# Performance work log

Hardware: AMD Instinct MI355X
Metric: run time of the kernel (lower is better)

Reference implementation:

```python
import jax, jax.numpy as jnp
import numpy as np

WINDOW_SIZE = 11
SIGMA = 1.5
C1 = 0.01 ** 2
C2 = 0.03 ** 2


def _gaussian_window(channels):
    coords = jnp.arange(WINDOW_SIZE, dtype=jnp.float32) - WINDOW_SIZE // 2
    g = jnp.exp(-coords ** 2 / (2.0 * SIGMA ** 2))
    g = g / g.sum()
    w2d = g[:, None] * g[None, :]                      # [K, K]
    # depthwise kernel: [out_ch=C, in_ch/groups=1, K, K]
    return jnp.broadcast_to(w2d[None, None], (channels, 1, WINDOW_SIZE, WINDOW_SIZE))


def _depthwise_conv(x, window):
    # x: [B, C, H, W]; grouped conv with feature_group_count = C, SAME padding
    C = x.shape[1]
    pad = WINDOW_SIZE // 2
    return jax.lax.conv_general_dilated(
        x, window,
        window_strides=(1, 1),
        padding=((pad, pad), (pad, pad)),
        dimension_numbers=("NCHW", "OIHW", "NCHW"),
        feature_group_count=C,
    )


def setup_inputs() -> dict:
    key = jax.random.key(0)
    k1, k2 = jax.random.split(key)
    shape = (16, 3, 512, 512)
    pred = jax.random.uniform(k1, shape, dtype=jnp.float32)
    target = jax.random.uniform(k2, shape, dtype=jnp.float32)
    return {"pred": pred, "target": target}


def reference(pred, target):
    C = pred.shape[1]
    window = _gaussian_window(C)
    mu_p = _depthwise_conv(pred, window)
    mu_t = _depthwise_conv(target, window)
    mu_p_sq = mu_p ** 2
    mu_t_sq = mu_t ** 2
    mu_cross = mu_p * mu_t
    sigma_p_sq = _depthwise_conv(pred ** 2, window) - mu_p_sq
    sigma_t_sq = _depthwise_conv(target ** 2, window) - mu_t_sq
    sigma_cross = _depthwise_conv(pred * target, window) - mu_cross
    ssim_map = ((2.0 * mu_cross + C1) * (2.0 * sigma_cross + C2)) / (
        (mu_p_sq + mu_t_sq + C1) * (sigma_p_sq + sigma_t_sq + C2)
    )
    return 1.0 - ssim_map.mean()
```

## Files before the change

kernel.cpp:

```cpp
#include <hip/hip_runtime.h>

#define HH 512
#define WW 512
#define NPLANE 48
#define BY 128
#define CHK 16
#define NCH (BY / CHK)
#define SLOTS 40
#define KS 11

typedef __attribute__((ext_vector_type(8))) short short8;
typedef __attribute__((ext_vector_type(4))) float floatx4;

__device__ inline unsigned pk2bf_rne(float a, float b) {
    union { float f; unsigned u; } ua, ub;
    ua.f = a; ub.f = b;
    unsigned lo = (ua.u + 0x7FFFu + ((ua.u >> 16) & 1u)) >> 16;
    unsigned hi = (ub.u + 0x7FFFu + ((ub.u >> 16) & 1u)) >> 16;
    return lo | (hi << 16);
}

#if defined(__has_builtin)
#if __has_builtin(__builtin_amdgcn_cvt_pk_bf16_f32)
#define HAVE_CVT_PK_BF16 1
#endif
#endif

__device__ inline unsigned pkbf(float a, float b) {
#ifdef HAVE_CVT_PK_BF16
    typedef __attribute__((ext_vector_type(2))) __bf16 bf16x2_t;
    bf16x2_t v = __builtin_amdgcn_cvt_pk_bf16_f32(a, b);
    return __builtin_bit_cast(unsigned, v);
#else
    union { float f; unsigned u; } ua, ub;
    ua.f = a; ub.f = b;
    return __builtin_amdgcn_perm(ub.u + 0x8000u, ua.u + 0x8000u, 0x07060302u);
#endif
}

struct Raw { float4 p0, p1, t0, t1; };

__global__ __launch_bounds__(256, 6) void ssim_kernel(
    const float* __restrict__ pred, const float* __restrict__ target,
    float* __restrict__ ws_sum)
{
    __shared__ __align__(16) short ring[4][5][16][SLOTS];
    __shared__ float red[4];

    const int tid = threadIdx.x;
    const int wv = tid >> 6;
    const int lane = tid & 63;
    const int m = lane & 15;
    const int quad = lane >> 4;

    float wsum = 0.f;
#pragma unroll
    for (int k = 0; k < KS; ++k) {
        float d = (float)(k - 5);
        wsum += __expf(-d * d * (1.0f / 4.5f));
    }
    const float invs = 1.0f / wsum;

    short8 Wf;
    {
        union { short8 v; unsigned u[4]; } W;
#pragma unroll
        for (int jj = 0; jj < 4; ++jj) {
            float v0, v1;
            {
                int idx = quad * 8 + 2 * jj - m - 3;
                float d = (float)(idx - 5);
                v0 = (idx >= 0 && idx < KS) ? __expf(-d * d * (1.0f / 4.5f)) * invs : 0.f;
            }
            {
                int idx = quad * 8 + 2 * jj + 1 - m - 3;
                float d = (float)(idx - 5);
                v1 = (idx >= 0 && idx < KS) ? __expf(-d * d * (1.0f / 4.5f)) * invs : 0.f;
            }
            W.u[jj] = pk2bf_rne(v0, v1);
        }
        Wf = W.v;
    }

    const size_t poff = (size_t)blockIdx.z * HH * WW;
    const float* __restrict__ pp = pred + poff;
    const float* __restrict__ tp = target + poff;
    const int X0 = blockIdx.x * 64 + wv * 16;
    const int rawX = X0 - 8;
    const int Y0 = blockIdx.y * BY;

    const float C1 = 1.0e-4f;
    const float C2 = 9.0e-4f;
    float lsum = 0.f;
    const floatx4 z = {0.f, 0.f, 0.f, 0.f};

    auto load_raw = [&](int k) -> Raw {
        Raw r;
        r.p0 = make_float4(0, 0, 0, 0); r.p1 = make_float4(0, 0, 0, 0);
        r.t0 = make_float4(0, 0, 0, 0); r.t1 = make_float4(0, 0, 0, 0);
        const int row = Y0 + CHK * k - 8 + m;
        if ((unsigned)row < (unsigned)HH) {
            const float* pr = pp + (size_t)row * WW;
            const float* tr = tp + (size_t)row * WW;
            const int c0 = rawX + quad * 8;
            if ((unsigned)c0 < (unsigned)WW) {
                r.p0 = *(const float4*)(pr + c0);
                r.t0 = *(const float4*)(tr + c0);
            }
            if ((unsigned)(c0 + 4) < (unsigned)WW) {
                r.p1 = *(const float4*)(pr + c0 + 4);
                r.t1 = *(const float4*)(tr + c0 + 4);
            }
        }
        return r;
    };

    auto h_step = [&](const Raw& r, int sb) {
        const float p[8] = {r.p0.x, r.p0.y, r.p0.z, r.p0.w,
                            r.p1.x, r.p1.y, r.p1.z, r.p1.w};
        const float t[8] = {r.t0.x, r.t0.y, r.t0.z, r.t0.w,
                            r.t1.x, r.t1.y, r.t1.z, r.t1.w};
        union { short8 v; unsigned u[4]; } Fp, Ft, Fpp, Ftt, Fpt;
#pragma unroll
        for (int jj = 0; jj < 4; ++jj) {
            const float a0 = p[2 * jj], a1 = p[2 * jj + 1];
            const float b0 = t[2 * jj], b1 = t[2 * jj + 1];
            Fp.u[jj]  = pkbf(a0, a1);
            Ft.u[jj]  = pkbf(b0, b1);
            Fpp.u[jj] = pkbf(a0 * a0, a1 * a1);
            Ftt.u[jj] = pkbf(b0 * b0, b1 * b1);
            Fpt.u[jj] = pkbf(a0 * b0, a1 * b1);
        }
        floatx4 Dp  = __builtin_amdgcn_mfma_f32_16x16x32_bf16(Fp.v,  Wf, z, 0, 0, 0);
        floatx4 Dt  = __builtin_amdgcn_mfma_f32_16x16x32_bf16(Ft.v,  Wf, z, 0, 0, 0);
        floatx4 Dpp = __builtin_amdgcn_mfma_f32_16x16x32_bf16(Fpp.v, Wf, z, 0, 0, 0);
        floatx4 Dtt = __builtin_amdgcn_mfma_f32_16x16x32_bf16(Ftt.v, Wf, z, 0, 0, 0);
        floatx4 Dpt = __builtin_amdgcn_mfma_f32_16x16x32_bf16(Fpt.v, Wf, z, 0, 0, 0);
        int slot = sb + quad * 4;
        if (slot >= SLOTS) slot -= SLOTS;
        uint2 v;
        v.x = pkbf(Dp[0], Dp[1]);   v.y = pkbf(Dp[2], Dp[3]);
        *(uint2*)&ring[wv][0][m][slot] = v;
        v.x = pkbf(Dt[0], Dt[1]);   v.y = pkbf(Dt[2], Dt[3]);
        *(uint2*)&ring[wv][1][m][slot] = v;
        v.x = pkbf(Dpp[0], Dpp[1]); v.y = pkbf(Dpp[2], Dpp[3]);
        *(uint2*)&ring[wv][2][m][slot] = v;
        v.x = pkbf(Dtt[0], Dtt[1]); v.y = pkbf(Dtt[2], Dtt[3]);
        *(uint2*)&ring[wv][3][m][slot] = v;
        v.x = pkbf(Dpt[0], Dpt[1]); v.y = pkbf(Dpt[2], Dpt[3]);
        *(uint2*)&ring[wv][4][m][slot] = v;
    };

    auto v_step = [&](int vb) {
        int sq = vb + quad * 8;
        if (sq >= SLOTS) sq -= SLOTS;
        const short8 Bp  = *(const short8*)&ring[wv][0][m][sq];
        const short8 Bt  = *(const short8*)&ring[wv][1][m][sq];
        const short8 Bpp = *(const short8*)&ring[wv][2][m][sq];
        const short8 Btt = *(const short8*)&ring[wv][3][m][sq];
        const short8 Bpt = *(const short8*)&ring[wv][4][m][sq];
        floatx4 Mp  = __builtin_amdgcn_mfma_f32_16x16x32_bf16(Wf, Bp,  z, 0, 0, 0);
        floatx4 Mt  = __builtin_amdgcn_mfma_f32_16x16x32_bf16(Wf, Bt,  z, 0, 0, 0);
        floatx4 Mpp = __builtin_amdgcn_mfma_f32_16x16x32_bf16(Wf, Bpp, z, 0, 0, 0);
        floatx4 Mtt = __builtin_amdgcn_mfma_f32_16x16x32_bf16(Wf, Btt, z, 0, 0, 0);
        floatx4 Mpt = __builtin_amdgcn_mfma_f32_16x16x32_bf16(Wf, Bpt, z, 0, 0, 0);
#pragma unroll
        for (int r = 0; r < 4; ++r) {
            const float mup = Mp[r], mut = Mt[r];
            const float mupsq = mup * mup, mutsq = mut * mut, mucr = mup * mut;
            const float sp2 = Mpp[r] - mupsq;
            const float st2 = Mtt[r] - mutsq;
            const float scr = Mpt[r] - mucr;
            const float n1 = 2.f * mucr + C1;
            const float n2 = 2.f * scr + C2;
            const float d1 = mupsq + mutsq + C1;
            const float d2 = sp2 + st2 + C2;
            lsum += __fdividef(n1 * n2, d1 * d2);
        }
    };

    Raw A = load_raw(0);
    Raw B = load_raw(1);
    int hb = SLOTS - 8;
    int vb = SLOTS - 8;
    h_step(A, hb);
    hb += CHK; if (hb >= SLOTS) hb -= SLOTS;
#pragma unroll 1
    for (int i = 0; i < NCH; ++i) {
        h_step(B, hb);
        hb += CHK; if (hb >= SLOTS) hb -= SLOTS;
        if (i + 2 <= NCH) B = load_raw(i + 2);
        v_step(vb);
        vb += CHK; if (vb >= SLOTS) vb -= SLOTS;
    }

#pragma unroll
    for (int off = 32; off > 0; off >>= 1) lsum += __shfl_down(lsum, off, 64);
    if (lane == 0) red[wv] = lsum;
    __syncthreads();
    if (tid == 0) {
        atomicAdd(ws_sum, red[0] + red[1] + red[2] + red[3]);
    }
}

__global__ void finalize_kernel(const float* __restrict__ ws_sum,
                                float* __restrict__ out) {
    out[0] = 1.0f - ws_sum[0] * (1.0f / 12582912.0f);
}

extern "C" void kernel_launch(void* const* d_in, const int* in_sizes, int n_in,
                              void* d_out, int out_size, void* d_ws, size_t ws_size,
                              hipStream_t stream) {
    const float* pred = (const float*)d_in[0];
    const float* target = (const float*)d_in[1];
    float* out = (float*)d_out;
    float* ws = (float*)d_ws;

    hipMemsetAsync(ws, 0, sizeof(float), stream);
    dim3 grid(WW / 64, HH / BY, NPLANE);
    ssim_kernel<<<grid, 256, 0, stream>>>(pred, target, ws);
    finalize_kernel<<<1, 1, 0, stream>>>(ws, out);
}
```

Before: 141.3 us.

## Deepen software pipeline so horizontal pass overlaps vertical MFMA and loads

```diff
diff --git a/kernel.cpp b/kernel.cpp
--- a/kernel.cpp
+++ b/kernel.cpp
@@ -11,6 +11,8 @@
 
 typedef __attribute__((ext_vector_type(8))) short short8;
 typedef __attribute__((ext_vector_type(4))) float floatx4;
+typedef __attribute__((ext_vector_type(2))) float float2v;
+typedef __attribute__((ext_vector_type(2))) __bf16 bf16x2v;
 
 __device__ inline unsigned pk2bf_rne(float a, float b) {
     union { float f; unsigned u; } ua, ub;
@@ -20,27 +22,15 @@
     return lo | (hi << 16);
 }
 
-#if defined(__has_builtin)
-#if __has_builtin(__builtin_amdgcn_cvt_pk_bf16_f32)
-#define HAVE_CVT_PK_BF16 1
-#endif
-#endif
-
 __device__ inline unsigned pkbf(float a, float b) {
-#ifdef HAVE_CVT_PK_BF16
-    typedef __attribute__((ext_vector_type(2))) __bf16 bf16x2_t;
-    bf16x2_t v = __builtin_amdgcn_cvt_pk_bf16_f32(a, b);
+    float2v f = {a, b};
+    bf16x2v v = __builtin_convertvector(f, bf16x2v);
     return __builtin_bit_cast(unsigned, v);
-#else
-    union { float f; unsigned u; } ua, ub;
-    ua.f = a; ub.f = b;
-    return __builtin_amdgcn_perm(ub.u + 0x8000u, ua.u + 0x8000u, 0x07060302u);
-#endif
 }
 
 struct Raw { float4 p0, p1, t0, t1; };
 
-__global__ __launch_bounds__(256, 6) void ssim_kernel(
+__global__ __launch_bounds__(256, 4) void ssim_kernel(
     const float* __restrict__ pred, const float* __restrict__ target,
     float* __restrict__ ws_sum)
 {
@@ -151,7 +141,15 @@
         *(uint2*)&ring[wv][4][m][slot] = v;
     };
 
-    auto v_step = [&](int vb) {
+    Raw A = load_raw(0);
+    Raw B = load_raw(1);
+    Raw C = load_raw(2);
+    h_step(A, (0 * CHK + SLOTS - 8) % SLOTS);
+    h_step(B, (1 * CHK + SLOTS - 8) % SLOTS);
+    int hb = (2 * CHK + SLOTS - 8) % SLOTS;
+    int vb = SLOTS - 8;
+#pragma unroll 1
+    for (int i = 0; i < NCH; ++i) {
         int sq = vb + quad * 8;
         if (sq >= SLOTS) sq -= SLOTS;
         const short8 Bp  = *(const short8*)&ring[wv][0][m][sq];
@@ -159,6 +157,14 @@
         const short8 Bpp = *(const short8*)&ring[wv][2][m][sq];
         const short8 Btt = *(const short8*)&ring[wv][3][m][sq];
         const short8 Bpt = *(const short8*)&ring[wv][4][m][sq];
+        vb += CHK; if (vb >= SLOTS) vb -= SLOTS;
+
+        if (i + 2 <= NCH) {
+            h_step(C, hb);
+            hb += CHK; if (hb >= SLOTS) hb -= SLOTS;
+        }
+        if (i + 3 <= NCH) C = load_raw(i + 3);
+
         floatx4 Mp  = __builtin_amdgcn_mfma_f32_16x16x32_bf16(Wf, Bp,  z, 0, 0, 0);
         floatx4 Mt  = __builtin_amdgcn_mfma_f32_16x16x32_bf16(Wf, Bt,  z, 0, 0, 0);
         floatx4 Mpp = __builtin_amdgcn_mfma_f32_16x16x32_bf16(Wf, Bpp, z, 0, 0, 0);
@@ -177,21 +183,6 @@
             const float d2 = sp2 + st2 + C2;
             lsum += __fdividef(n1 * n2, d1 * d2);
         }
-    };
-
-    Raw A = load_raw(0);
-    Raw B = load_raw(1);
-    int hb = SLOTS - 8;
-    int vb = SLOTS - 8;
-    h_step(A, hb);
-    hb += CHK; if (hb >= SLOTS) hb -= SLOTS;
-#pragma unroll 1
-    for (int i = 0; i < NCH; ++i) {
-        h_step(B, hb);
-        hb += CHK; if (hb >= SLOTS) hb -= SLOTS;
-        if (i + 2 <= NCH) B = load_raw(i + 2);
-        v_step(vb);
-        vb += CHK; if (vb >= SLOTS) vb -= SLOTS;
     }
 
 #pragma unroll
```

New measurement: 140.3 us. Within noise of the previous version (-0.7%).
